# Performance work log

Measured on AMD Instinct MI355X. Metric: run time of the kernel, lower is better.

## Reference

```python
import jax, jax.numpy as jnp
import numpy as np

N = 50000
E = 1600000
IN = 128
HID = 128
OUT = 64
NL = 200000
NEG_SLOPE = 0.2


def _glorot(key, shape):
    fan_in, fan_out = shape[0], shape[-1]
    s = jnp.sqrt(6.0 / (fan_in + fan_out))
    return jax.random.uniform(key, shape, jnp.float32, -s, s)


def setup_inputs() -> dict:
    key = jax.random.key(0)
    ks = jax.random.split(key, 16)
    x = jax.random.normal(ks[0], (N, IN), jnp.float32)
    edge_index = jax.random.randint(ks[1], (2, E), 0, N, dtype=jnp.int32)
    edge_label_index = jax.random.randint(ks[2], (2, NL), 0, N, dtype=jnp.int32)
    return {
        "x": x,
        "edge_index": edge_index,
        "edge_label_index": edge_label_index,
        "W1": _glorot(ks[3], (IN, HID)),  "a1s": _glorot(ks[4], (HID,)),  "a1d": _glorot(ks[5], (HID,)),  "b1": jnp.zeros((HID,), jnp.float32),
        "W2": _glorot(ks[6], (HID, HID)), "a2s": _glorot(ks[7], (HID,)),  "a2d": _glorot(ks[8], (HID,)),  "b2": jnp.zeros((HID,), jnp.float32),
        "W3": _glorot(ks[9], (HID, HID)), "a3s": _glorot(ks[10], (HID,)), "a3d": _glorot(ks[11], (HID,)), "b3": jnp.zeros((HID,), jnp.float32),
        "W4": _glorot(ks[12], (HID, OUT)), "b4": jnp.zeros((OUT,), jnp.float32),
    }


def _add_self_loops(edge_index, n):
    loop = jnp.arange(n, dtype=edge_index.dtype)
    return jnp.concatenate([edge_index, jnp.stack([loop, loop])], axis=1)


def gat_conv(x, edge_index, W, a_s, a_d, b):
    """PyG GATConv, heads=1, add_self_loops=True: gather, LeakyReLU score,
    segment softmax over destination nodes, scatter-add aggregate."""
    n = x.shape[0]
    ei = _add_self_loops(edge_index, n)
    src, dst = ei[0], ei[1]
    h = x @ W                                    # [N, H]
    e = jax.nn.leaky_relu((h @ a_s)[src] + (h @ a_d)[dst], NEG_SLOPE)  # [E']
    m = jax.ops.segment_max(e, dst, num_segments=n)
    p = jnp.exp(e - m[dst])
    s = jax.ops.segment_sum(p, dst, num_segments=n)
    alpha = p / s[dst]                           # segment softmax
    out = jax.ops.segment_sum(h[src] * alpha[:, None], dst, num_segments=n)
    return out + b


def gcn_conv(x, edge_index, W, b):
    """PyG GCNConv: self-loops + symmetric degree normalization."""
    n = x.shape[0]
    ei = _add_self_loops(edge_index, n)
    src, dst = ei[0], ei[1]
    h = x @ W
    deg = jax.ops.segment_sum(jnp.ones(src.shape, h.dtype), dst, num_segments=n)
    dinv = jax.lax.rsqrt(deg)
    norm = dinv[src] * dinv[dst]                 # [E']
    out = jax.ops.segment_sum(h[src] * norm[:, None], dst, num_segments=n)
    return out + b


def reference(x, edge_index, edge_label_index,
              W1, a1s, a1d, b1, W2, a2s, a2d, b2,
              W3, a3s, a3d, b3, W4, b4):
    h = jax.nn.relu(gat_conv(x, edge_index, W1, a1s, a1d, b1))
    h = jax.nn.relu(gat_conv(h, edge_index, W2, a2s, a2d, b2))
    h = jax.nn.relu(gat_conv(h, edge_index, W3, a3s, a3d, b3))
    z = gcn_conv(h, edge_index, W4, b4)          # [N, OUT]
    # decode: dot product of endpoint embeddings -> link logits [NL]
    return (z[edge_label_index[0]] * z[edge_label_index[1]]).sum(axis=-1)
```

## Files before the change

### kernel.cpp

```cpp
#include <hip/hip_runtime.h>
#include <hip/hip_fp16.h>
#include <math.h>

#define NN   50000
#define NE   1600000
#define DHID 128
#define DOUTC 64
#define NLBL 200000
#define CAP  80
#define NEG  0.2f
#define NBK  196
#define CAPB 8800
#define CHK  4096

typedef unsigned short u16;
typedef _Float16 half8 __attribute__((ext_vector_type(8)));
typedef float floatx4 __attribute__((ext_vector_type(4)));


__global__ __launch_bounds__(256) void k_bin(const int* __restrict__ ei,
                                             int* __restrict__ gcnt,
                                             unsigned* __restrict__ bins) {
    __shared__ int cntL[NBK];
    __shared__ int curL[NBK];
    const int tid = threadIdx.x;
    const int e0 = blockIdx.x * CHK + tid * 16;
    const bool act = (e0 + 15) < NE;

    unsigned pk[16];
    int bb[16];
    if (act) {
#pragma unroll
        for (int g = 0; g < 4; ++g) {
            int4 s4 = *(const int4*)&ei[e0 + g * 4];
            int4 d4 = *(const int4*)&ei[NE + e0 + g * 4];
            int sa[4] = {s4.x, s4.y, s4.z, s4.w};
            int da[4] = {d4.x, d4.y, d4.z, d4.w};
#pragma unroll
            for (int k = 0; k < 4; ++k) {
                int idx = g * 4 + k;
                bb[idx] = da[k] >> 8;
                pk[idx] = (unsigned)sa[k] | ((unsigned)(da[k] & 255) << 16);
            }
        }
    }
    for (int i = tid; i < NBK; i += 256) cntL[i] = 0;
    __syncthreads();
    if (act) {
#pragma unroll
        for (int k = 0; k < 16; ++k) atomicAdd(&cntL[bb[k]], 1);
    }
    __syncthreads();
    for (int i = tid; i < NBK; i += 256) curL[i] = atomicAdd(&gcnt[i], cntL[i]);
    __syncthreads();
    if (act) {
#pragma unroll
        for (int k = 0; k < 16; ++k) {
            int off = atomicAdd(&curL[bb[k]], 1);
            bins[(size_t)bb[k] * CAPB + off] = pk[k];
        }
    }
}

__global__ __launch_bounds__(256) void k_build(const unsigned* __restrict__ bins,
                                               const int* __restrict__ gcnt,
                                               int* __restrict__ cnt,
                                               u16* __restrict__ csr) {
    __shared__ u16 rows[256 * CAP];
    __shared__ int cur[256];
    const int b = blockIdx.x, tid = threadIdx.x;
    const int d0 = b << 8;
    const int nd = min(256, NN - d0);
    if (tid < nd) { cur[tid] = 1; rows[tid * CAP] = (u16)(d0 + tid); }
    __syncthreads();
    const int n = gcnt[b];
    for (int i = tid; i < n; i += 256) {
        unsigned v = bins[(size_t)b * CAPB + i];
        int s = v & 0xFFFF, dl = v >> 16;
        int pos = atomicAdd(&cur[dl], 1);
        if (pos < CAP) rows[dl * CAP + pos] = (u16)s;
    }
    __syncthreads();
    const unsigned* rw = (const unsigned*)rows;
    unsigned* cw = (unsigned*)(csr + (size_t)d0 * CAP);
    const int tot = nd * (CAP / 2);
    for (int i = tid; i < tot; i += 256) cw[i] = rw[i];
    if (tid < nd) cnt[d0 + tid] = cur[tid];
}


__global__ __launch_bounds__(256) void k_prep_w(const float* __restrict__ W1f,
                                                const float* __restrict__ W2f,
                                                const float* __restrict__ W3f,
                                                const float* __restrict__ W4f,
                                                half8* __restrict__ Wf1,
                                                half8* __restrict__ Wf2,
                                                half8* __restrict__ Wf3,
                                                half8* __restrict__ Wf4,
                                                int* __restrict__ gcnt) {
    if (blockIdx.x == 28) {
        int i = threadIdx.x;
        if (i < NBK) gcnt[i] = 0;
        return;
    }
    int e = blockIdx.x * 256 + threadIdx.x;
    const float* W;
    half8* Wf;
    int nout, le;
    if (e < 2048)      { W = W1f; Wf = Wf1; nout = 128; le = e; }
    else if (e < 4096) { W = W2f; Wf = Wf2; nout = 128; le = e - 2048; }
    else if (e < 6144) { W = W3f; Wf = Wf3; nout = 128; le = e - 4096; }
    else               { W = W4f; Wf = Wf4; nout = 64;  le = e - 6144; }
    int c = le >> 8, rem = le & 255, ks = rem >> 6, lane = rem & 63;
    int n = lane & 15, quad = lane >> 4;
    int col = c * 16 + n, k0 = ks * 32 + quad * 8;
    half8 v;
#pragma unroll
    for (int j = 0; j < 8; ++j) v[j] = (_Float16)W[(size_t)(k0 + j) * nout + col];
    Wf[le] = v;
}


template <int NOUT, bool ATTN, typename TA>
__global__ __launch_bounds__(256) void gemm_mfma(const TA* __restrict__ A0,
                                                 const TA* __restrict__ A1,
                                                 const half8* __restrict__ Wf,
                                                 __half* __restrict__ C0,
                                                 __half* __restrict__ C1,
                                                 const float* __restrict__ a_s,
                                                 const float* __restrict__ a_d,
                                                 float* __restrict__ asv,
                                                 float* __restrict__ adv, int M) {
    constexpr int CT = NOUT / 16;
    const int tid = threadIdx.x;
    const int wave = tid >> 6, lane = tid & 63;
    const int n = lane & 15, quad = lane >> 4;
    const int row0 = blockIdx.x * 64 + wave * 16;

    const int row = row0 + n;
    const bool ok = row < M;
    half8 a[4];
    half8 zz = {};
#pragma unroll
    for (int ks = 0; ks < 4; ++ks) {
        if (!ok) { a[ks] = zz; continue; }
        int c128 = ks * 32 + quad * 8;
        if constexpr (sizeof(TA) == 2) {
            const TA* Ah = (c128 < 64) ? A0 : A1;
            a[ks] = *(const half8*)((const _Float16*)Ah + (size_t)row * 64 + (c128 & 63));
        } else {
            const float* Ap = (const float*)A0 + (size_t)row * 128 + c128;
            float4 f0 = *(const float4*)Ap;
            float4 f1 = *(const float4*)(Ap + 4);
            half8 v;
            v[0] = (_Float16)f0.x; v[1] = (_Float16)f0.y; v[2] = (_Float16)f0.z; v[3] = (_Float16)f0.w;
            v[4] = (_Float16)f1.x; v[5] = (_Float16)f1.y; v[6] = (_Float16)f1.z; v[7] = (_Float16)f1.w;
            a[ks] = v;
        }
    }

    floatx4 acc[CT];
#pragma unroll
    for (int c = 0; c < CT; ++c) acc[c] = (floatx4){0.f, 0.f, 0.f, 0.f};

#pragma unroll
    for (int c = 0; c < CT; ++c) {
#pragma unroll
        for (int ks = 0; ks < 4; ++ks) {
            half8 b = Wf[(c * 4 + ks) * 64 + lane];
            acc[c] = __builtin_amdgcn_mfma_f32_16x16x32_f16(b, a[ks], acc[c], 0, 0, 0);
        }
    }

    if (ok) {
#pragma unroll
        for (int c = 0; c < CT; ++c) {
            __half* Ch = (NOUT == 64 || c < 4) ? C0 : C1;
            int coff = (NOUT == 64 || c < 4) ? c * 16 : (c - 4) * 16;
            __half2 h0 = __floats2half2_rn(acc[c][0], acc[c][1]);
            __half2 h1 = __floats2half2_rn(acc[c][2], acc[c][3]);
            uint2 u;
            __builtin_memcpy(&u.x, &h0, 4);
            __builtin_memcpy(&u.y, &h1, 4);
            *(uint2*)&Ch[(size_t)row * 64 + coff + quad * 4] = u;
        }
    }

    if (ATTN) {
        float ps = 0.f, pd = 0.f;
#pragma unroll
        for (int c = 0; c < CT; ++c) {
#pragma unroll
            for (int reg = 0; reg < 4; ++reg) {
                float w = acc[c][reg];
                ps = fmaf(w, a_s[c * 16 + quad * 4 + reg], ps);
                pd = fmaf(w, a_d[c * 16 + quad * 4 + reg], pd);
            }
        }
        ps += __shfl_xor(ps, 16); ps += __shfl_xor(ps, 32);
        pd += __shfl_xor(pd, 16); pd += __shfl_xor(pd, 32);
        if (quad == 0 && ok) { asv[row] = ps; adv[row] = pd; }
    }
}

__device__ inline void fma_h8v(half8 h, float al, float* acc) {
#pragma unroll
    for (int k = 0; k < 8; ++k) acc[k] = fmaf(al, (float)h[k], acc[k]);
}


__global__ __launch_bounds__(256) void k_gat_agg(const __half* __restrict__ h0,
                                                 const __half* __restrict__ h1,
                                                 const int* __restrict__ cnt,
                                                 const u16* __restrict__ csr,
                                                 const float* __restrict__ asv,
                                                 const float* __restrict__ adv,
                                                 const float* __restrict__ bias,
                                                 __half* __restrict__ out0,
                                                 __half* __restrict__ out1) {
    __shared__ float alsL[4][88];
    __shared__ int   srcL[4][88];
    int lane = threadIdx.x & 63, wv = threadIdx.x >> 6;
    int d = blockIdx.x * 4 + wv;
    if (d >= NN) return;
    int deg = cnt[d]; if (deg > CAP) deg = CAP;
    const float advd = adv[d];
    const u16* rowp = csr + (size_t)d * CAP;

    int j0 = lane, j1 = lane + 64;
    int s0 = 0, s1 = 0;
    float e0 = -INFINITY, e1 = -INFINITY;
    if (j0 < deg) {
        s0 = rowp[j0];
        float t = asv[s0] + advd;
        e0 = (t >= 0.f) ? t : NEG * t;
    }
    if (j1 < deg) {
        s1 = rowp[j1];
        float t = asv[s1] + advd;
        e1 = (t >= 0.f) ? t : NEG * t;
    }
    float m = fmaxf(e0, e1);
#pragma unroll
    for (int off = 32; off; off >>= 1) m = fmaxf(m, __shfl_xor(m, off));
    float p0 = (j0 < deg) ? __expf(e0 - m) : 0.f;
    float p1 = (j1 < deg) ? __expf(e1 - m) : 0.f;
    float s = p0 + p1;
#pragma unroll
    for (int off = 32; off; off >>= 1) s += __shfl_xor(s, off);
    float inv = 1.f / s;
    alsL[wv][j0] = p0 * inv;
    srcL[wv][j0] = s0;
    if (j1 < 88) { alsL[wv][j1] = p1 * inv; srcL[wv][j1] = s1; }

    int slot = lane >> 3, r = lane & 7;
    int degp = (deg + 7) & ~7;
#pragma unroll
    for (int half = 0; half < 2; ++half) {
        const __half* ht = half ? h1 : h0;
        __half* ot = half ? out1 : out0;
        float acc[8];
#pragma unroll
        for (int k = 0; k < 8; ++k) acc[k] = 0.f;

        for (int base = 0; base < degp; base += 8) {
            int idx = base + slot;
            float al = alsL[wv][idx];
            int   sj = srcL[wv][idx];
            half8 hv = *(const half8*)&ht[(size_t)sj * 64 + r * 8];
            fma_h8v(hv, al, acc);
        }
#pragma unroll
        for (int k = 0; k < 8; ++k) {
            acc[k] += __shfl_xor(acc[k], 8);
            acc[k] += __shfl_xor(acc[k], 16);
            acc[k] += __shfl_xor(acc[k], 32);
        }
        if (slot == 0) {
            __half2 ho[4];
#pragma unroll
            for (int k = 0; k < 4; ++k) {
                float oa = fmaxf(acc[2 * k]     + bias[half * 64 + r * 8 + 2 * k],     0.f);
                float ob = fmaxf(acc[2 * k + 1] + bias[half * 64 + r * 8 + 2 * k + 1], 0.f);
                ho[k] = __floats2half2_rn(oa, ob);
            }
            uint4 u;
            __builtin_memcpy(&u, &ho[0], 16);
            *(uint4*)&ot[(size_t)d * 64 + r * 8] = u;
        }
    }
}


__global__ __launch_bounds__(256) void k_gcn_agg(const __half* __restrict__ h,
                                                 const int* __restrict__ cnt,
                                                 const u16* __restrict__ csr,
                                                 const float* __restrict__ bias,
                                                 __half* __restrict__ z) {
    __shared__ float nmL[4][88];
    __shared__ int   srcL[4][88];
    int lane = threadIdx.x & 63, wv = threadIdx.x >> 6;
    int d = blockIdx.x * 4 + wv;
    if (d >= NN) return;
    int degc = cnt[d];
    int deg = degc > CAP ? CAP : degc;
    float did = rsqrtf((float)degc);
    const u16* rowp = csr + (size_t)d * CAP;

    int j0 = lane, j1 = lane + 64;
    int s0 = 0, s1 = 0;
    float n0 = 0.f, n1 = 0.f;
    if (j0 < deg) { s0 = rowp[j0]; n0 = rsqrtf((float)cnt[s0]) * did; }
    if (j1 < deg) { s1 = rowp[j1]; n1 = rsqrtf((float)cnt[s1]) * did; }
    nmL[wv][j0] = n0;
    srcL[wv][j0] = s0;
    if (j1 < 88) { nmL[wv][j1] = n1; srcL[wv][j1] = s1; }

    int slot = lane >> 3, r = lane & 7;
    float acc[8];
#pragma unroll
    for (int k = 0; k < 8; ++k) acc[k] = 0.f;

    int degp = (deg + 7) & ~7;
    for (int base = 0; base < degp; base += 8) {
        int idx = base + slot;
        float nm = nmL[wv][idx];
        int   sj = srcL[wv][idx];
        half8 hv = *(const half8*)&h[(size_t)sj * 64 + r * 8];
        fma_h8v(hv, nm, acc);
    }
#pragma unroll
    for (int k = 0; k < 8; ++k) {
        acc[k] += __shfl_xor(acc[k], 8);
        acc[k] += __shfl_xor(acc[k], 16);
        acc[k] += __shfl_xor(acc[k], 32);
    }
    if (slot == 0) {
        __half2 ho[4];
#pragma unroll
        for (int k = 0; k < 4; ++k) {
            float oa = acc[2 * k]     + bias[r * 8 + 2 * k];
            float ob = acc[2 * k + 1] + bias[r * 8 + 2 * k + 1];
            ho[k] = __floats2half2_rn(oa, ob);
        }
        uint4 u;
        __builtin_memcpy(&u, &ho[0], 16);
        *(uint4*)&z[(size_t)d * 64 + r * 8] = u;
    }
}


__global__ __launch_bounds__(256) void k_decode(const __half* __restrict__ z,
                                                const int* __restrict__ eli,
                                                float* __restrict__ outp) {
    int lane = threadIdx.x & 63, wv = threadIdx.x >> 6;
    int g = lane >> 4, r = lane & 15;
    int idx = (blockIdx.x * 4 + wv) * 4 + g;
    if (idx >= NLBL) return;
    int a = eli[idx], b = eli[NLBL + idx];
    uint2 ua = *(const uint2*)&z[(size_t)a * 64 + r * 4];
    uint2 ub = *(const uint2*)&z[(size_t)b * 64 + r * 4];
    float2 a0 = __half22float2(*(__half2*)&ua.x);
    float2 a1 = __half22float2(*(__half2*)&ua.y);
    float2 b0 = __half22float2(*(__half2*)&ub.x);
    float2 b1 = __half22float2(*(__half2*)&ub.y);
    float v = a0.x * b0.x + a0.y * b0.y + a1.x * b1.x + a1.y * b1.y;
#pragma unroll
    for (int off = 8; off; off >>= 1) v += __shfl_xor(v, off);
    if (r == 0) outp[idx] = v;
}


extern "C" void kernel_launch(void* const* d_in, const int* in_sizes, int n_in,
                              void* d_out, int out_size, void* d_ws, size_t ws_size,
                              hipStream_t stream) {
    const float* x   = (const float*)d_in[0];
    const int*   ei  = (const int*)d_in[1];
    const int*   eli = (const int*)d_in[2];
    const float* W1 = (const float*)d_in[3];
    const float* a1s = (const float*)d_in[4];
    const float* a1d = (const float*)d_in[5];
    const float* b1 = (const float*)d_in[6];
    const float* W2 = (const float*)d_in[7];
    const float* a2s = (const float*)d_in[8];
    const float* a2d = (const float*)d_in[9];
    const float* b2 = (const float*)d_in[10];
    const float* W3 = (const float*)d_in[11];
    const float* a3s = (const float*)d_in[12];
    const float* a3d = (const float*)d_in[13];
    const float* b3 = (const float*)d_in[14];
    const float* W4 = (const float*)d_in[15];
    const float* b4 = (const float*)d_in[16];
    float* outp = (float*)d_out;

    char* p = (char*)d_ws;
    auto alloc = [&](size_t bytes) -> char* {
        char* r = p;
        p += (bytes + 255) & ~(size_t)255;
        return r;
    };
    int*    cnt  = (int*)alloc((size_t)NN * 4);
    u16*    csr  = (u16*)alloc((size_t)NN * CAP * 2);
    int*    gcnt = (int*)alloc((size_t)NBK * 4);
    float*  asv  = (float*)alloc((size_t)NN * 4);
    float*  advv = (float*)alloc((size_t)NN * 4);
    __half* G0   = (__half*)alloc((size_t)NN * 64 * 2);
    __half* G1   = (__half*)alloc((size_t)NN * 64 * 2);
    __half* B1a  = (__half*)alloc((size_t)NN * 64 * 2);
    __half* B1b  = (__half*)alloc((size_t)NN * 64 * 2);
    __half* B2a  = (__half*)alloc((size_t)NN * 64 * 2);
    __half* B2b  = (__half*)alloc((size_t)NN * 64 * 2);
    __half* zf   = (__half*)alloc((size_t)NN * 64 * 2);
    half8*  Wf1  = (half8*)alloc(2048 * 16);
    half8*  Wf2  = (half8*)alloc(2048 * 16);
    half8*  Wf3  = (half8*)alloc(2048 * 16);
    half8*  Wf4  = (half8*)alloc(1024 * 16);
    unsigned* bins = (unsigned*)alloc((size_t)NBK * CAPB * 4);

    const int gBin  = (NE + CHK - 1) / CHK;
    const int gGemm = (NN + 63) / 64;
    const int gNode = (NN + 3) / 4;
    const int gDec  = (NLBL + 15) / 16;

    k_prep_w<<<29, 256, 0, stream>>>(W1, W2, W3, W4, Wf1, Wf2, Wf3, Wf4, gcnt);
    k_bin<<<gBin, 256, 0, stream>>>(ei, gcnt, bins);
    k_build<<<NBK, 256, 0, stream>>>(bins, gcnt, cnt, csr);

    gemm_mfma<128, true, float><<<gGemm, 256, 0, stream>>>(x, x, Wf1, G0, G1, a1s, a1d, asv, advv, NN);
    k_gat_agg<<<gNode, 256, 0, stream>>>(G0, G1, cnt, csr, asv, advv, b1, B1a, B1b);

    gemm_mfma<128, true, __half><<<gGemm, 256, 0, stream>>>(B1a, B1b, Wf2, G0, G1, a2s, a2d, asv, advv, NN);
    k_gat_agg<<<gNode, 256, 0, stream>>>(G0, G1, cnt, csr, asv, advv, b2, B2a, B2b);

    gemm_mfma<128, true, __half><<<gGemm, 256, 0, stream>>>(B2a, B2b, Wf3, G0, G1, a3s, a3d, asv, advv, NN);
    k_gat_agg<<<gNode, 256, 0, stream>>>(G0, G1, cnt, csr, asv, advv, b3, B1a, B1b);

    gemm_mfma<64, false, __half><<<gGemm, 256, 0, stream>>>(B1a, B1b, Wf4, G0, G0, nullptr, nullptr, nullptr, nullptr, NN);
    k_gcn_agg<<<gNode, 256, 0, stream>>>(G0, cnt, csr, b4, zf);

    k_decode<<<gDec, 256, 0, stream>>>(zf, eli, outp);
}
```

Before: 388.1 us.

## Split node features into 32-column planes for cache-friendlier gathers

Feature matrices are now stored as four 32-column fp16 planes (two for the 64-wide GCN layer) instead of two 64-column halves. The GEMM and the aggregation kernels index these planes, so each gather pass touches a smaller per-plane working set that fits better in L2/LLC. Each wave now covers 16 neighbours per step with 4 lanes per row, which adds one more shuffle round to the reduction. GAT outputs are written with nontemporal stores. In exchange there are more passes over the neighbour list per node and smaller 64-byte row segments per gather.

```diff
diff --git a/kernel.cpp b/kernel.cpp
--- a/kernel.cpp
+++ b/kernel.cpp
@@ -16,6 +16,7 @@
 typedef unsigned short u16;
 typedef _Float16 half8 __attribute__((ext_vector_type(8)));
 typedef float floatx4 __attribute__((ext_vector_type(4)));
+typedef unsigned int u32x4 __attribute__((ext_vector_type(4)));
 
 
 __global__ __launch_bounds__(256) void k_bin(const int* __restrict__ ei,
@@ -124,9 +125,13 @@
 template <int NOUT, bool ATTN, typename TA>
 __global__ __launch_bounds__(256) void gemm_mfma(const TA* __restrict__ A0,
                                                  const TA* __restrict__ A1,
+                                                 const TA* __restrict__ A2,
+                                                 const TA* __restrict__ A3,
                                                  const half8* __restrict__ Wf,
                                                  __half* __restrict__ C0,
                                                  __half* __restrict__ C1,
+                                                 __half* __restrict__ C2,
+                                                 __half* __restrict__ C3,
                                                  const float* __restrict__ a_s,
                                                  const float* __restrict__ a_d,
                                                  float* __restrict__ asv,
@@ -137,6 +142,9 @@
     const int n = lane & 15, quad = lane >> 4;
     const int row0 = blockIdx.x * 64 + wave * 16;
 
+    const TA* Aq[4] = {A0, A1, A2, A3};
+    __half* Cq[4] = {C0, C1, C2, C3};
+
     const int row = row0 + n;
     const bool ok = row < M;
     half8 a[4];
@@ -144,12 +152,10 @@
 #pragma unroll
     for (int ks = 0; ks < 4; ++ks) {
         if (!ok) { a[ks] = zz; continue; }
-        int c128 = ks * 32 + quad * 8;
         if constexpr (sizeof(TA) == 2) {
-            const TA* Ah = (c128 < 64) ? A0 : A1;
-            a[ks] = *(const half8*)((const _Float16*)Ah + (size_t)row * 64 + (c128 & 63));
+            a[ks] = *(const half8*)((const _Float16*)Aq[ks] + (size_t)row * 32 + quad * 8);
         } else {
-            const float* Ap = (const float*)A0 + (size_t)row * 128 + c128;
+            const float* Ap = (const float*)A0 + (size_t)row * 128 + ks * 32 + quad * 8;
             float4 f0 = *(const float4*)Ap;
             float4 f1 = *(const float4*)(Ap + 4);
             half8 v;
@@ -175,14 +181,12 @@
     if (ok) {
 #pragma unroll
         for (int c = 0; c < CT; ++c) {
-            __half* Ch = (NOUT == 64 || c < 4) ? C0 : C1;
-            int coff = (NOUT == 64 || c < 4) ? c * 16 : (c - 4) * 16;
             __half2 h0 = __floats2half2_rn(acc[c][0], acc[c][1]);
             __half2 h1 = __floats2half2_rn(acc[c][2], acc[c][3]);
             uint2 u;
             __builtin_memcpy(&u.x, &h0, 4);
             __builtin_memcpy(&u.y, &h1, 4);
-            *(uint2*)&Ch[(size_t)row * 64 + coff + quad * 4] = u;
+            *(uint2*)&Cq[c >> 1][(size_t)row * 32 + (c & 1) * 16 + quad * 4] = u;
         }
     }
 
@@ -211,13 +215,17 @@
 
 __global__ __launch_bounds__(256) void k_gat_agg(const __half* __restrict__ h0,
                                                  const __half* __restrict__ h1,
+                                                 const __half* __restrict__ h2,
+                                                 const __half* __restrict__ h3,
                                                  const int* __restrict__ cnt,
                                                  const u16* __restrict__ csr,
                                                  const float* __restrict__ asv,
                                                  const float* __restrict__ adv,
                                                  const float* __restrict__ bias,
-                                                 __half* __restrict__ out0,
-                                                 __half* __restrict__ out1) {
+                                                 __half* __restrict__ o0,
+                                                 __half* __restrict__ o1,
+                                                 __half* __restrict__ o2,
+                                                 __half* __restrict__ o3) {
     __shared__ float alsL[4][88];
     __shared__ int   srcL[4][88];
     int lane = threadIdx.x & 63, wv = threadIdx.x >> 6;
@@ -253,25 +261,27 @@
     srcL[wv][j0] = s0;
     if (j1 < 88) { alsL[wv][j1] = p1 * inv; srcL[wv][j1] = s1; }
 
-    int slot = lane >> 3, r = lane & 7;
-    int degp = (deg + 7) & ~7;
-#pragma unroll
-    for (int half = 0; half < 2; ++half) {
-        const __half* ht = half ? h1 : h0;
-        __half* ot = half ? out1 : out0;
+    const __half* hq[4] = {h0, h1, h2, h3};
+    __half* oq[4] = {o0, o1, o2, o3};
+    int slot = lane >> 2, r = lane & 3;
+    int degp = (deg + 15) & ~15;
+#pragma unroll
+    for (int q = 0; q < 4; ++q) {
+        const __half* ht = hq[q];
         float acc[8];
 #pragma unroll
         for (int k = 0; k < 8; ++k) acc[k] = 0.f;
 
-        for (int base = 0; base < degp; base += 8) {
+        for (int base = 0; base < degp; base += 16) {
             int idx = base + slot;
             float al = alsL[wv][idx];
             int   sj = srcL[wv][idx];
-            half8 hv = *(const half8*)&ht[(size_t)sj * 64 + r * 8];
+            half8 hv = *(const half8*)&ht[(size_t)sj * 32 + r * 8];
             fma_h8v(hv, al, acc);
         }
 #pragma unroll
         for (int k = 0; k < 8; ++k) {
+            acc[k] += __shfl_xor(acc[k], 4);
             acc[k] += __shfl_xor(acc[k], 8);
             acc[k] += __shfl_xor(acc[k], 16);
             acc[k] += __shfl_xor(acc[k], 32);
@@ -280,19 +290,20 @@
             __half2 ho[4];
 #pragma unroll
             for (int k = 0; k < 4; ++k) {
-                float oa = fmaxf(acc[2 * k]     + bias[half * 64 + r * 8 + 2 * k],     0.f);
-                float ob = fmaxf(acc[2 * k + 1] + bias[half * 64 + r * 8 + 2 * k + 1], 0.f);
+                float oa = fmaxf(acc[2 * k]     + bias[q * 32 + r * 8 + 2 * k],     0.f);
+                float ob = fmaxf(acc[2 * k + 1] + bias[q * 32 + r * 8 + 2 * k + 1], 0.f);
                 ho[k] = __floats2half2_rn(oa, ob);
             }
-            uint4 u;
+            u32x4 u;
             __builtin_memcpy(&u, &ho[0], 16);
-            *(uint4*)&ot[(size_t)d * 64 + r * 8] = u;
-        }
-    }
-}
-
-
-__global__ __launch_bounds__(256) void k_gcn_agg(const __half* __restrict__ h,
+            __builtin_nontemporal_store(u, (u32x4*)&oq[q][(size_t)d * 32 + r * 8]);
+        }
+    }
+}
+
+
+__global__ __launch_bounds__(256) void k_gcn_agg(const __half* __restrict__ h0,
+                                                 const __half* __restrict__ h1,
                                                  const int* __restrict__ cnt,
                                                  const u16* __restrict__ csr,
                                                  const float* __restrict__ bias,
@@ -316,36 +327,42 @@
     srcL[wv][j0] = s0;
     if (j1 < 88) { nmL[wv][j1] = n1; srcL[wv][j1] = s1; }
 
-    int slot = lane >> 3, r = lane & 7;
-    float acc[8];
-#pragma unroll
-    for (int k = 0; k < 8; ++k) acc[k] = 0.f;
-
-    int degp = (deg + 7) & ~7;
-    for (int base = 0; base < degp; base += 8) {
-        int idx = base + slot;
-        float nm = nmL[wv][idx];
-        int   sj = srcL[wv][idx];
-        half8 hv = *(const half8*)&h[(size_t)sj * 64 + r * 8];
-        fma_h8v(hv, nm, acc);
-    }
-#pragma unroll
-    for (int k = 0; k < 8; ++k) {
-        acc[k] += __shfl_xor(acc[k], 8);
-        acc[k] += __shfl_xor(acc[k], 16);
-        acc[k] += __shfl_xor(acc[k], 32);
-    }
-    if (slot == 0) {
-        __half2 ho[4];
-#pragma unroll
-        for (int k = 0; k < 4; ++k) {
-            float oa = acc[2 * k]     + bias[r * 8 + 2 * k];
-            float ob = acc[2 * k + 1] + bias[r * 8 + 2 * k + 1];
-            ho[k] = __floats2half2_rn(oa, ob);
-        }
-        uint4 u;
-        __builtin_memcpy(&u, &ho[0], 16);
-        *(uint4*)&z[(size_t)d * 64 + r * 8] = u;
+    const __half* hq[2] = {h0, h1};
+    int slot = lane >> 2, r = lane & 3;
+    int degp = (deg + 15) & ~15;
+#pragma unroll
+    for (int q = 0; q < 2; ++q) {
+        const __half* ht = hq[q];
+        float acc[8];
+#pragma unroll
+        for (int k = 0; k < 8; ++k) acc[k] = 0.f;
+
+        for (int base = 0; base < degp; base += 16) {
+            int idx = base + slot;
+            float nm = nmL[wv][idx];
+            int   sj = srcL[wv][idx];
+            half8 hv = *(const half8*)&ht[(size_t)sj * 32 + r * 8];
+            fma_h8v(hv, nm, acc);
+        }
+#pragma unroll
+        for (int k = 0; k < 8; ++k) {
+            acc[k] += __shfl_xor(acc[k], 4);
+            acc[k] += __shfl_xor(acc[k], 8);
+            acc[k] += __shfl_xor(acc[k], 16);
+            acc[k] += __shfl_xor(acc[k], 32);
+        }
+        if (slot == 0) {
+            __half2 ho[4];
+#pragma unroll
+            for (int k = 0; k < 4; ++k) {
+                float oa = acc[2 * k]     + bias[q * 32 + r * 8 + 2 * k];
+                float ob = acc[2 * k + 1] + bias[q * 32 + r * 8 + 2 * k + 1];
+                ho[k] = __floats2half2_rn(oa, ob);
+            }
+            uint4 u;
+            __builtin_memcpy(&u, &ho[0], 16);
+            *(uint4*)&z[(size_t)d * 64 + q * 32 + r * 8] = u;
+        }
     }
 }
 
@@ -404,12 +421,10 @@
     int*    gcnt = (int*)alloc((size_t)NBK * 4);
     float*  asv  = (float*)alloc((size_t)NN * 4);
     float*  advv = (float*)alloc((size_t)NN * 4);
-    __half* G0   = (__half*)alloc((size_t)NN * 64 * 2);
-    __half* G1   = (__half*)alloc((size_t)NN * 64 * 2);
-    __half* B1a  = (__half*)alloc((size_t)NN * 64 * 2);
-    __half* B1b  = (__half*)alloc((size_t)NN * 64 * 2);
-    __half* B2a  = (__half*)alloc((size_t)NN * 64 * 2);
-    __half* B2b  = (__half*)alloc((size_t)NN * 64 * 2);
+    __half* Gq[4], *B1q[4], *B2q[4];
+    for (int q = 0; q < 4; ++q) Gq[q]  = (__half*)alloc((size_t)NN * 32 * 2);
+    for (int q = 0; q < 4; ++q) B1q[q] = (__half*)alloc((size_t)NN * 32 * 2);
+    for (int q = 0; q < 4; ++q) B2q[q] = (__half*)alloc((size_t)NN * 32 * 2);
     __half* zf   = (__half*)alloc((size_t)NN * 64 * 2);
     half8*  Wf1  = (half8*)alloc(2048 * 16);
     half8*  Wf2  = (half8*)alloc(2048 * 16);
@@ -426,17 +441,25 @@
     k_bin<<<gBin, 256, 0, stream>>>(ei, gcnt, bins);
     k_build<<<NBK, 256, 0, stream>>>(bins, gcnt, cnt, csr);
 
-    gemm_mfma<128, true, float><<<gGemm, 256, 0, stream>>>(x, x, Wf1, G0, G1, a1s, a1d, asv, advv, NN);
-    k_gat_agg<<<gNode, 256, 0, stream>>>(G0, G1, cnt, csr, asv, advv, b1, B1a, B1b);
-
-    gemm_mfma<128, true, __half><<<gGemm, 256, 0, stream>>>(B1a, B1b, Wf2, G0, G1, a2s, a2d, asv, advv, NN);
-    k_gat_agg<<<gNode, 256, 0, stream>>>(G0, G1, cnt, csr, asv, advv, b2, B2a, B2b);
-
-    gemm_mfma<128, true, __half><<<gGemm, 256, 0, stream>>>(B2a, B2b, Wf3, G0, G1, a3s, a3d, asv, advv, NN);
-    k_gat_agg<<<gNode, 256, 0, stream>>>(G0, G1, cnt, csr, asv, advv, b3, B1a, B1b);
-
-    gemm_mfma<64, false, __half><<<gGemm, 256, 0, stream>>>(B1a, B1b, Wf4, G0, G0, nullptr, nullptr, nullptr, nullptr, NN);
-    k_gcn_agg<<<gNode, 256, 0, stream>>>(G0, cnt, csr, b4, zf);
+    gemm_mfma<128, true, float><<<gGemm, 256, 0, stream>>>(
+        x, x, x, x, Wf1, Gq[0], Gq[1], Gq[2], Gq[3], a1s, a1d, asv, advv, NN);
+    k_gat_agg<<<gNode, 256, 0, stream>>>(Gq[0], Gq[1], Gq[2], Gq[3], cnt, csr, asv, advv, b1,
+                                         B1q[0], B1q[1], B1q[2], B1q[3]);
+
+    gemm_mfma<128, true, __half><<<gGemm, 256, 0, stream>>>(
+        B1q[0], B1q[1], B1q[2], B1q[3], Wf2, Gq[0], Gq[1], Gq[2], Gq[3], a2s, a2d, asv, advv, NN);
+    k_gat_agg<<<gNode, 256, 0, stream>>>(Gq[0], Gq[1], Gq[2], Gq[3], cnt, csr, asv, advv, b2,
+                                         B2q[0], B2q[1], B2q[2], B2q[3]);
+
+    gemm_mfma<128, true, __half><<<gGemm, 256, 0, stream>>>(
+        B2q[0], B2q[1], B2q[2], B2q[3], Wf3, Gq[0], Gq[1], Gq[2], Gq[3], a3s, a3d, asv, advv, NN);
+    k_gat_agg<<<gNode, 256, 0, stream>>>(Gq[0], Gq[1], Gq[2], Gq[3], cnt, csr, asv, advv, b3,
+                                         B1q[0], B1q[1], B1q[2], B1q[3]);
+
+    gemm_mfma<64, false, __half><<<gGemm, 256, 0, stream>>>(
+        B1q[0], B1q[1], B1q[2], B1q[3], Wf4, Gq[0], Gq[1], Gq[0], Gq[1],
+        nullptr, nullptr, nullptr, nullptr, NN);
+    k_gcn_agg<<<gNode, 256, 0, stream>>>(Gq[0], Gq[1], cnt, csr, b4, zf);
 
     k_decode<<<gDec, 256, 0, stream>>>(zf, eli, outp);
 }
```

After: 520.7 us. +34.1%, slower.
